# Performance work log

Measured on AMD Instinct MI355X. Metric: run time of the kernel, lower is better.

Reference implementation:

```python
import jax, jax.numpy as jnp
import numpy as np

N = 1_000_000          # total nodes
C = 128                # in_channels
NUM_SEGMENTS = 10_000  # number of graphs (= batch.max()+1 in the torch code)


def setup_inputs() -> dict:
    key = jax.random.key(0)
    k1, k2, k3 = jax.random.split(key, 3)
    x = jax.random.normal(k1, (N, C), dtype=jnp.float32)
    batch = jnp.sort(jax.random.randint(k2, (N,), 0, NUM_SEGMENTS, dtype=jnp.int64))
    W = jax.random.normal(k3, (C, 1), dtype=jnp.float32) * (1.0 / np.sqrt(C))
    b = jnp.zeros((1,), dtype=jnp.float32)
    return {"x": x, "batch": batch, "W": W, "b": b}


def reference(x, batch, W, b):
    # attention score: Linear(C->1) followed by Softmax over dim=1 (a size-1
    # axis in the original torch code, so the softmax yields all ones; we
    # faithfully reproduce that math).
    logits = x @ W + b                       # [N, 1]
    score = jax.nn.softmax(logits, axis=1)   # [N, 1] (== ones)
    weighted = score * x                     # [N, C]
    # scatter_add keyed by batch -> per-graph sum
    out = jax.ops.segment_sum(weighted, batch, num_segments=NUM_SEGMENTS)  # [G, C]
    return out
```

## Files before the change

### kernel.cpp

```cpp
#include <hip/hip_runtime.h>


#define C 128
#define ROWS_PER_WAVE 128
#define WAVES_PER_BLOCK 4
#define BLOCK_THREADS (WAVES_PER_BLOCK * 64)
#define UNROLL 4

typedef float f4 __attribute__((ext_vector_type(4)));

__device__ __forceinline__ void flush_acc(float* __restrict__ out, int seg,
                                          int col4, f4& acc) {
    float* o = out + (size_t)seg * C + 4 * col4;
    atomicAdd(o + 0, acc.x);
    atomicAdd(o + 1, acc.y);
    atomicAdd(o + 2, acc.z);
    atomicAdd(o + 3, acc.w);
    acc = (f4){0.f, 0.f, 0.f, 0.f};
}

__global__ __launch_bounds__(BLOCK_THREADS)
void segsum_kernel(const f4* __restrict__ xv,
                   const int* __restrict__ batch,
                   float* __restrict__ out,
                   int n_rows, int n_segs) {
    const int wave = blockIdx.x * WAVES_PER_BLOCK + (threadIdx.x >> 6);
    const int lane = threadIdx.x & 63;
    const int half = lane >> 5;
    const int col4 = lane & 31;

    long row0 = (long)wave * ROWS_PER_WAVE;
    if (row0 >= n_rows) return;
    long row_end = row0 + ROWS_PER_WAVE;
    if (row_end > n_rows) row_end = n_rows;

    f4 acc = (f4){0.f, 0.f, 0.f, 0.f};
    long first = row0 + half;
    if (first > n_rows - 1) first = n_rows - 1;
    int cur = batch[first];
    cur = min(max(cur, 0), n_segs - 1);

    long r = row0;
    for (; r + 2 * UNROLL <= row_end; r += 2 * UNROLL) {
        f4  v[UNROLL];
        int seg[UNROLL];
#pragma unroll
        for (int j = 0; j < UNROLL; ++j) {
            long row = r + 2 * j + half;
            v[j] = __builtin_nontemporal_load(xv + row * (C / 4) + col4);
            int2 b2 = *(const int2*)(batch + r + 2 * j);
            int  s  = half ? b2.y : b2.x;
            seg[j] = min(max(s, 0), n_segs - 1);
        }
#pragma unroll
        for (int j = 0; j < UNROLL; ++j) {
            if (seg[j] != cur) {
                flush_acc(out, cur, col4, acc);
                cur = seg[j];
            }
            acc += v[j];
        }
    }
    for (; r + 1 < row_end; r += 2) {
        long row = r + half;
        f4 v = __builtin_nontemporal_load(xv + row * (C / 4) + col4);
        int2 b2 = *(const int2*)(batch + r);
        int  s  = half ? b2.y : b2.x;
        s = min(max(s, 0), n_segs - 1);
        if (s != cur) {
            flush_acc(out, cur, col4, acc);
            cur = s;
        }
        acc += v;
    }
    flush_acc(out, cur, col4, acc);
}

extern "C" void kernel_launch(void* const* d_in, const int* in_sizes, int n_in,
                              void* d_out, int out_size, void* d_ws, size_t ws_size,
                              hipStream_t stream) {
    const float* x     = (const float*)d_in[0];
    const int*   batch = (const int*)d_in[1];
    float* out = (float*)d_out;

    const int n_rows = in_sizes[0] / C;
    const int n_segs = out_size / C;

    hipMemsetAsync(d_out, 0, (size_t)out_size * sizeof(float), stream);

    const int n_waves  = (n_rows + ROWS_PER_WAVE - 1) / ROWS_PER_WAVE;
    const int n_blocks = (n_waves + WAVES_PER_BLOCK - 1) / WAVES_PER_BLOCK;

    segsum_kernel<<<n_blocks, BLOCK_THREADS, 0, stream>>>(
        (const f4*)x, batch, out, n_rows, n_segs);
}
```

Before: 647.5 us.

## Preload segment ids per wave and broadcast via shuffles; halve rows per wave

Each lane now loads one batch index for the wave's 64 rows up front, and segment ids are fetched with cross-lane shuffles instead of per-iteration global int2 loads. Rows per wave drop to 64 and the unroll doubles to 8, which doubles the wave count and puts more loads in flight. An odd-row tail case is added. The cost is more waves and more boundary flush atomics per segment.

```diff
diff --git a/kernel.cpp b/kernel.cpp
--- a/kernel.cpp
+++ b/kernel.cpp
@@ -2,10 +2,10 @@
 
 
 #define C 128
-#define ROWS_PER_WAVE 128
+#define ROWS_PER_WAVE 64
 #define WAVES_PER_BLOCK 4
 #define BLOCK_THREADS (WAVES_PER_BLOCK * 64)
-#define UNROLL 4
+#define UNROLL 8
 
 typedef float f4 __attribute__((ext_vector_type(4)));
 
@@ -33,45 +33,53 @@
     if (row0 >= n_rows) return;
     long row_end = row0 + ROWS_PER_WAVE;
     if (row_end > n_rows) row_end = n_rows;
+    const int nrows_w = (int)(row_end - row0);
+
+    long bidx = row0 + lane;
+    if (bidx > (long)n_rows - 1) bidx = (long)n_rows - 1;
+    int bval = batch[bidx];
+    bval = min(max(bval, 0), n_segs - 1);
 
     f4 acc = (f4){0.f, 0.f, 0.f, 0.f};
-    long first = row0 + half;
-    if (first > n_rows - 1) first = n_rows - 1;
-    int cur = batch[first];
-    cur = min(max(cur, 0), n_segs - 1);
+    int cur = __shfl(bval, half);
 
-    long r = row0;
-    for (; r + 2 * UNROLL <= row_end; r += 2 * UNROLL) {
-        f4  v[UNROLL];
-        int seg[UNROLL];
+    const f4* base = xv + row0 * (C / 4) + col4;
+
+    int i = 0;
+    for (; i + 2 * UNROLL <= nrows_w; i += 2 * UNROLL) {
+        f4 v[UNROLL];
+#pragma unroll
+        for (int j = 0; j < UNROLL; ++j)
+            v[j] = __builtin_nontemporal_load(base + (long)(i + 2 * j + half) * (C / 4));
 #pragma unroll
         for (int j = 0; j < UNROLL; ++j) {
-            long row = r + 2 * j + half;
-            v[j] = __builtin_nontemporal_load(xv + row * (C / 4) + col4);
-            int2 b2 = *(const int2*)(batch + r + 2 * j);
-            int  s  = half ? b2.y : b2.x;
-            seg[j] = min(max(s, 0), n_segs - 1);
-        }
-#pragma unroll
-        for (int j = 0; j < UNROLL; ++j) {
-            if (seg[j] != cur) {
+            int seg = __shfl(bval, i + 2 * j + half);
+            if (seg != cur) {
                 flush_acc(out, cur, col4, acc);
-                cur = seg[j];
+                cur = seg;
             }
             acc += v[j];
         }
     }
-    for (; r + 1 < row_end; r += 2) {
-        long row = r + half;
-        f4 v = __builtin_nontemporal_load(xv + row * (C / 4) + col4);
-        int2 b2 = *(const int2*)(batch + r);
-        int  s  = half ? b2.y : b2.x;
-        s = min(max(s, 0), n_segs - 1);
-        if (s != cur) {
+    for (; i + 1 < nrows_w; i += 2) {
+        f4 v = __builtin_nontemporal_load(base + (long)(i + half) * (C / 4));
+        int seg = __shfl(bval, i + half);
+        if (seg != cur) {
             flush_acc(out, cur, col4, acc);
-            cur = s;
+            cur = seg;
         }
         acc += v;
+    }
+    if (i < nrows_w) {
+        int seg = __shfl(bval, i);
+        if (half == 0) {
+            f4 v = __builtin_nontemporal_load(base + (long)i * (C / 4));
+            if (seg != cur) {
+                flush_acc(out, cur, col4, acc);
+                cur = seg;
+            }
+            acc += v;
+        }
     }
     flush_acc(out, cur, col4, acc);
 }
```

After: 657.6 us. About the same (+1.6%).
